# Kernel optimization log

Measured on AMD Instinct MI355X. Metric: run time of the kernel, lower is better.

## Reference

```python
import jax, jax.numpy as jnp
import numpy as np

H = 64
IN_DIM = 32
N = 50000
E = 100000
B = 500


def setup_inputs() -> dict:
    key = jax.random.key(0)
    ks = jax.random.split(key, 16)
    def rn(k, shape, s=0.05):
        return jax.random.normal(k, shape, dtype=jnp.float32) * s
    inp = dict(
        nfeat=rn(ks[0], (N, IN_DIM), 1.0),
        efeat=rn(ks[1], (E, 5), 1.0),
        lin0_w=rn(ks[2], (IN_DIM, H)), lin0_b=jnp.zeros((H,), jnp.float32),
        ew1=rn(ks[3], (5, 128)), eb1=jnp.zeros((128,), jnp.float32),
        ew2=rn(ks[4], (128, H * H)), eb2=jnp.zeros((H * H,), jnp.float32),
        conv_b=jnp.zeros((H,), jnp.float32),
        gru_wih=rn(ks[5], (3 * H, H)), gru_whh=rn(ks[6], (3 * H, H)),
        gru_bih=jnp.zeros((3 * H,), jnp.float32), gru_bhh=jnp.zeros((3 * H,), jnp.float32),
        lstm_wih=rn(ks[7], (4 * H, 2 * H)), lstm_whh=rn(ks[8], (4 * H, H)),
        lstm_bih=jnp.zeros((4 * H,), jnp.float32), lstm_bhh=jnp.zeros((4 * H,), jnp.float32),
        fc1_w=rn(ks[9], (2 * H, H)), fc1_b=jnp.zeros((H,), jnp.float32),
        fc2_w=rn(ks[10], (H, 1)), fc2_b=jnp.zeros((1,), jnp.float32),
        src=jax.random.randint(ks[11], (E,), 0, N),
        dst=jax.random.randint(ks[12], (E,), 0, N),
        graph_id=jnp.arange(N) // (N // B),  # B graphs of equal size, sorted
        num_graphs=B,
    )
    return inp


def reference(nfeat, efeat, lin0_w, lin0_b, ew1, eb1, ew2, eb2, conv_b,
              gru_wih, gru_whh, gru_bih, gru_bhh,
              lstm_wih, lstm_whh, lstm_bih, lstm_bhh,
              fc1_w, fc1_b, fc2_w, fc2_b,
              src, dst, graph_id, num_graphs):
    n_nodes = nfeat.shape[0]
    # lin0 + relu
    h = jax.nn.relu(nfeat @ lin0_w + lin0_b)  # [N, H]
    # edge-conditioned weight matrices (same for all 3 iterations)
    We = (jax.nn.relu(efeat @ ew1 + eb1) @ ew2 + eb2).reshape(-1, H, H)  # [E, H, H]
    deg = jnp.maximum(
        jax.ops.segment_sum(jnp.ones(src.shape[0], jnp.float32), dst, num_segments=n_nodes), 1.0)
    for _ in range(3):
        # NNConv: gather src feats, per-edge matmul, scatter-mean at dst
        msg = jnp.einsum('eh,eho->eo', h[src], We)  # [E, H]
        agg = jax.ops.segment_sum(msg, dst, num_segments=n_nodes) / deg[:, None]
        m = jax.nn.relu(agg + conv_b)
        # GRU step (PyTorch gate order r,z,n)
        gi = m @ gru_wih.T + gru_bih
        gh = h @ gru_whh.T + gru_bhh
        r = jax.nn.sigmoid(gi[:, :H] + gh[:, :H])
        z = jax.nn.sigmoid(gi[:, H:2 * H] + gh[:, H:2 * H])
        n = jnp.tanh(gi[:, 2 * H:] + r * gh[:, 2 * H:])
        h = (1.0 - z) * n + z * h
    feat = h  # [N, H]
    # Set2Set pooling: 3 iters, 1-layer LSTM with input 2H
    q_star = jnp.zeros((num_graphs, 2 * H), jnp.float32)
    hh = jnp.zeros((num_graphs, H), jnp.float32)
    cc = jnp.zeros((num_graphs, H), jnp.float32)
    for _ in range(3):
        gates = q_star @ lstm_wih.T + lstm_bih + hh @ lstm_whh.T + lstm_bhh
        i = jax.nn.sigmoid(gates[:, :H])
        f = jax.nn.sigmoid(gates[:, H:2 * H])
        g = jnp.tanh(gates[:, 2 * H:3 * H])
        o = jax.nn.sigmoid(gates[:, 3 * H:])
        cc = f * cc + i * g
        hh = o * jnp.tanh(cc)
        q = hh  # [B, H]
        e = jnp.sum(feat * q[graph_id], axis=-1)  # [N]
        emax = jax.ops.segment_max(e, graph_id, num_segments=num_graphs)
        alpha = jnp.exp(e - emax[graph_id])
        denom = jax.ops.segment_sum(alpha, graph_id, num_segments=num_graphs)
        alpha = alpha / denom[graph_id]
        readout = jax.ops.segment_sum(alpha[:, None] * feat, graph_id, num_segments=num_graphs)
        q_star = jnp.concatenate([q, readout], axis=-1)  # [B, 2H]
    pred = jax.nn.relu(q_star @ fc1_w + fc1_b) @ fc2_w + fc2_b  # [B, 1]
    return pred.reshape(-1)
```

## Files before the change

### kernel.cpp

```cpp
#include <hip/hip_runtime.h>

#define HD 64
#define NNODE 50000
#define NEDGE 100000
#define NGR 500
#define NPG 100
#define EPAD 100352
#define NCH 66
#define NUPL 65

typedef _Float16 f16;
typedef _Float16 f16x2 __attribute__((ext_vector_type(2)));
typedef _Float16 f16x8 __attribute__((ext_vector_type(8)));
typedef float f32x4 __attribute__((ext_vector_type(4)));

__device__ __forceinline__ float sigmoidf_(float x) { return 1.f / (1.f + __expf(-x)); }

__device__ __forceinline__ void gload16(const void* g, void* l) {
    __builtin_amdgcn_global_load_lds((const __attribute__((address_space(1))) unsigned int*)g,
                                     (__attribute__((address_space(3))) unsigned int*)l, 16, 0, 0);
}

#define G_NODE 12500
#define G_EMLP 392
#define G_GRU  48
#define G_T1   128
#define G_T2   64
#define G_IDX  392
#define G_ALL (G_NODE + G_EMLP + G_GRU + G_T1 + G_T2 + G_IDX)

__global__ __launch_bounds__(256) void k_prep_all(
    const float* __restrict__ nfeat, const float* __restrict__ lin0_w, const float* __restrict__ lin0_b,
    const float* __restrict__ efeat, const float* __restrict__ ew1, const float* __restrict__ eb1,
    const float* __restrict__ gwih, const float* __restrict__ gwhh,
    const float* __restrict__ lwih, const float* __restrict__ lwhh,
    const int* __restrict__ src, const int* __restrict__ dst,
    float* __restrict__ h, f16x2* __restrict__ uP,
    f16* __restrict__ gB1, f16* __restrict__ gB2,
    float* __restrict__ lwihT, float* __restrict__ lwhhT,
    int* __restrict__ srcP, int* __restrict__ dstP, int* __restrict__ cnt) {
    int bb = blockIdx.x;
    int t = threadIdx.x;
    if (bb < G_NODE) {
        int idx = bb * 256 + t;
        int n = idx >> 6, o = idx & 63;
        if (n >= NNODE) return;
        const float* nf = nfeat + n * 32;
        float acc = lin0_b[o];
#pragma unroll
        for (int i = 0; i < 32; i++) acc += nf[i] * lin0_w[i * 64 + o];
        h[idx] = fmaxf(acc, 0.f);
        return;
    }
    bb -= G_NODE;
    if (bb < G_EMLP) {
        __shared__ float sw[5 * 128];
        __shared__ float sb[128];
        for (int idx = t; idx < 640; idx += 256) sw[idx] = ew1[idx];
        if (t < 128) sb[t] = eb1[t];
        __syncthreads();
        int e = bb * 256 + t;
        bool valid = e < NEDGE;
        float ef[5];
#pragma unroll
        for (int i = 0; i < 5; i++) ef[i] = valid ? efeat[e * 5 + i] : 0.f;
#pragma unroll 2
        for (int c = 0; c < 64; c++) {
            float v[2];
#pragma unroll
            for (int s = 0; s < 2; s++) {
                int k = 2 * c + s;
                float acc = sb[k];
#pragma unroll
                for (int i = 0; i < 5; i++) acc += ef[i] * sw[i * 128 + k];
                v[s] = valid ? fmaxf(acc, 0.f) : 0.f;
            }
            f16x2 pv;
            pv[0] = (f16)v[0];
            pv[1] = (f16)v[1];
            uP[(size_t)c * EPAD + e] = pv;
        }
        {
            f16x2 pv;
            pv[0] = valid ? (f16)1.f : (f16)0.f;
            pv[1] = pv[0];
            uP[(size_t)64 * EPAD + e] = pv;
        }
        return;
    }
    bb -= G_EMLP;
    if (bb < G_GRU) {
        int idx = bb * 256 + t;
        int cp = idx >> 6, k = idx & 63;
        int w = cp / 48, rem = cp % 48;
        int tg = rem >> 4, cc = rem & 15;
        int orow = tg * 64 + w * 16 + cc;
        gB1[idx] = (f16)gwih[orow * 64 + k];
        gB2[idx] = (f16)gwhh[orow * 64 + k];
        return;
    }
    bb -= G_GRU;
    if (bb < G_T1) {
        int idx = bb * 256 + t;
        int r = idx >> 7, c = idx & 127;
        lwihT[c * 256 + r] = lwih[idx];
        return;
    }
    bb -= G_T1;
    if (bb < G_T2) {
        int idx = bb * 256 + t;
        int r = idx >> 6, c = idx & 63;
        lwhhT[c * 256 + r] = lwhh[idx];
        return;
    }
    bb -= G_T2;
    {
        int e = bb * 256 + t;
        if (e >= EPAD) return;
        if (e < NEDGE) {
            int d = dst[e];
            srcP[e] = src[e];
            dstP[e] = d;
            atomicAdd(&cnt[d], 1);
        } else {
            srcP[e] = 0;
            dstP[e] = -1;
        }
    }
}

__global__ __launch_bounds__(256) void k_pack_b(const float* __restrict__ ew2,
                                                const float* __restrict__ eb2,
                                                f16* __restrict__ w2hp) {
    __shared__ float s[8192];
    int c = blockIdx.x, t = threadIdx.x;
    for (int i = t; i < 8192; i += 256) {
        int kg = c * 128 + (i >> 6);
        float v = 0.f;
        if (kg < 8192) v = ew2[(size_t)c * 8192 + i];
        else if (kg < 8256) v = eb2[(kg - 8192) * 64 + (i & 63)];
        s[i] = v;
    }
    __syncthreads();
    f16* outp = w2hp + (size_t)c * 8192 + t * 32;
#pragma unroll
    for (int ff = 0; ff < 4; ff++) {
        int F = t * 4 + ff;
        int l = F & 63;
        int jj = (F >> 6) & 3;
        int sl = (F >> 8) & 3;
        f16x8 v;
#pragma unroll
        for (int q = 0; q < 8; q++)
            v[q] = (f16)s[(sl * 32 + ((l >> 4) << 3) + q) * 64 + jj * 16 + (l & 15)];
        *(f16x8*)(outp + ff * 8) = v;
    }
}

__global__ __launch_bounds__(256) void k_msg(
    const float* __restrict__ h, const f16x2* __restrict__ uP, const f16* __restrict__ w2hp,
    const int* __restrict__ srcP, const int* __restrict__ dstP, float* __restrict__ agg) {
    __shared__ __attribute__((aligned(16))) f16 sB[2 * 8192];
    int t = threadIdx.x;
    int w = t >> 6, l = t & 63;
    int eb = blockIdx.x * 256 + w * 64;
    int lr = l & 15, lg = l >> 4;
    f16x8 xf[4][2];
#pragma unroll
    for (int i = 0; i < 4; i++) {
        const float* xb = h + (size_t)srcP[eb + i * 16 + lr] * 64;
#pragma unroll
        for (int p = 0; p < 2; p++) {
            float4 v0 = *(const float4*)(xb + p * 32 + lg * 8);
            float4 v1 = *(const float4*)(xb + p * 32 + lg * 8 + 4);
            f16x8 xv;
            xv[0] = (f16)v0.x; xv[1] = (f16)v0.y; xv[2] = (f16)v0.z; xv[3] = (f16)v0.w;
            xv[4] = (f16)v1.x; xv[5] = (f16)v1.y; xv[6] = (f16)v1.z; xv[7] = (f16)v1.w;
            xf[i][p] = xv;
        }
    }
    const f16x8* gB = (const f16x8*)w2hp;
    f16x8* sB8 = (f16x8*)sB;
#pragma unroll
    for (int i = 0; i < 4; i++)
        gload16(gB + i * 256 + w * 64 + l, sB8 + i * 256 + w * 64 + l);
    f32x4 acc[4][4];
#pragma unroll
    for (int i = 0; i < 4; i++)
#pragma unroll
        for (int j = 0; j < 4; j++) acc[i][j] = (f32x4){0.f, 0.f, 0.f, 0.f};
    f16x2 uc[4], un[4];
#pragma unroll
    for (int i = 0; i < 4; i++) uc[i] = uP[eb + i * 16 + lr];
    __syncthreads();
#pragma unroll 1
    for (int c = 0; c <= 64; c++) {
        int buf = c & 1;
        if (c < 64) {
            const f16x8* gs = gB + (size_t)(c + 1) * 1024;
            f16x8* ld = sB8 + (buf ^ 1) * 1024;
#pragma unroll
            for (int i = 0; i < 4; i++)
                gload16(gs + i * 256 + w * 64 + l, ld + i * 256 + w * 64 + l);
            int cn = c + 1;
#pragma unroll
            for (int i = 0; i < 4; i++) un[i] = uP[(size_t)cn * EPAD + eb + i * 16 + lr];
        }
        f16x8 bf[4][4];
#pragma unroll
        for (int s = 0; s < 4; s++)
#pragma unroll
            for (int j = 0; j < 4; j++)
                bf[s][j] = sB8[buf * 1024 + s * 256 + j * 64 + l];
        __builtin_amdgcn_s_setprio(1);
#pragma unroll
        for (int s = 0; s < 4; s++) {
#pragma unroll
            for (int i = 0; i < 4; i++) {
                f16x8 av = xf[i][s & 1] * uc[i][s >> 1];
#pragma unroll
                for (int j = 0; j < 4; j++)
                    acc[i][j] = __builtin_amdgcn_mfma_f32_16x16x32_f16(av, bf[s][j], acc[i][j], 0, 0, 0);
            }
        }
        __builtin_amdgcn_s_setprio(0);
#pragma unroll
        for (int i = 0; i < 4; i++) uc[i] = un[i];
        __syncthreads();
    }
#pragma unroll
    for (int i = 0; i < 4; i++) {
        int rb = eb + i * 16 + lg * 4;
        int4 d4 = *(const int4*)(dstP + rb);
#pragma unroll
        for (int r = 0; r < 4; r++) {
            int d = (r == 0) ? d4.x : (r == 1) ? d4.y : (r == 2) ? d4.z : d4.w;
            if (d >= 0) {
                float* ap = agg + (size_t)d * 64 + lr;
#pragma unroll
                for (int j = 0; j < 4; j++) atomicAdd(ap + j * 16, acc[i][j][r]);
            }
        }
    }
}

#define GWP 72
__global__ __launch_bounds__(256) void k_gru2(float* __restrict__ agg,
                                              const int* __restrict__ cnt,
                                              const float* __restrict__ convb,
                                              const f16* __restrict__ B1g,
                                              const f16* __restrict__ B2g,
                                              const float* __restrict__ bih,
                                              const float* __restrict__ bhh,
                                              float* __restrict__ h) {
    __shared__ f16 sM[64 * GWP];
    __shared__ f16 sH[64 * GWP];
    int t = threadIdx.x;
    int nb = blockIdx.x * 64;
    int w = t >> 6, l = t & 63, lr = l & 15, lg = l >> 4;
    f16x8 b1[2][3], b2[2][3];
#pragma unroll
    for (int kk = 0; kk < 2; kk++)
#pragma unroll
        for (int j = 0; j < 3; j++) {
            size_t off = (size_t)(w * 48 + j * 16 + lr) * 64 + kk * 32 + lg * 8;
            b1[kk][j] = *(const f16x8*)(B1g + off);
            b2[kk][j] = *(const f16x8*)(B2g + off);
        }
#pragma unroll
    for (int it = 0; it < 16; it++) {
        int idx = t + 256 * it;
        int node = idx >> 6, k = idx & 63;
        int gn = nb + node;
        float mv = 0.f, hv = 0.f;
        if (gn < NNODE) {
            size_t off = (size_t)gn * 64 + k;
            float dinv = 1.f / (float)max(cnt[gn], 1);
            mv = fmaxf(agg[off] * dinv + convb[k], 0.f);
            hv = h[off];
            agg[off] = 0.f;
        }
        sM[node * GWP + k] = (f16)mv;
        sH[node * GWP + k] = (f16)hv;
    }
    __syncthreads();
    f32x4 aih[4][3], ahh[4][3];
#pragma unroll
    for (int i = 0; i < 4; i++)
#pragma unroll
        for (int j = 0; j < 3; j++) {
            aih[i][j] = (f32x4){0.f, 0.f, 0.f, 0.f};
            ahh[i][j] = (f32x4){0.f, 0.f, 0.f, 0.f};
        }
#pragma unroll
    for (int kk = 0; kk < 2; kk++) {
        f16x8 am[4], ah[4];
#pragma unroll
        for (int i = 0; i < 4; i++) {
            am[i] = *(const f16x8*)(sM + (i * 16 + lr) * GWP + kk * 32 + lg * 8);
            ah[i] = *(const f16x8*)(sH + (i * 16 + lr) * GWP + kk * 32 + lg * 8);
        }
#pragma unroll
        for (int i = 0; i < 4; i++)
#pragma unroll
            for (int j = 0; j < 3; j++) {
                aih[i][j] = __builtin_amdgcn_mfma_f32_16x16x32_f16(am[i], b1[kk][j], aih[i][j], 0, 0, 0);
                ahh[i][j] = __builtin_amdgcn_mfma_f32_16x16x32_f16(ah[i], b2[kk][j], ahh[i][j], 0, 0, 0);
            }
    }
    float bi0 = bih[0 * 64 + w * 16 + lr], bh0 = bhh[0 * 64 + w * 16 + lr];
    float bi1 = bih[1 * 64 + w * 16 + lr], bh1 = bhh[1 * 64 + w * 16 + lr];
    float bi2 = bih[2 * 64 + w * 16 + lr], bh2 = bhh[2 * 64 + w * 16 + lr];
#pragma unroll
    for (int i = 0; i < 4; i++)
#pragma unroll
        for (int r = 0; r < 4; r++) {
            int node = i * 16 + lg * 4 + r;
            int gn = nb + node;
            if (gn >= NNODE) continue;
            float rg = sigmoidf_(aih[i][0][r] + bi0 + ahh[i][0][r] + bh0);
            float z = sigmoidf_(aih[i][1][r] + bi1 + ahh[i][1][r] + bh1);
            float nn = tanhf(aih[i][2][r] + bi2 + rg * (ahh[i][2][r] + bh2));
            size_t off = (size_t)gn * 64 + w * 16 + lr;
            float hold = h[off];
            h[off] = (1.f - z) * nn + z * hold;
        }
}

#define FP 68
__global__ __launch_bounds__(256) void k_s2s(const float* __restrict__ feat,
                                             const float* __restrict__ wihT,
                                             const float* __restrict__ whhT,
                                             const float* __restrict__ lbih,
                                             const float* __restrict__ lbhh,
                                             const float* __restrict__ fc1w,
                                             const float* __restrict__ fc1b,
                                             const float* __restrict__ fc2w,
                                             const float* __restrict__ fc2b,
                                             float* __restrict__ out) {
    __shared__ float sf[NPG * FP];
    __shared__ float sq[128];
    __shared__ float sh[64], scc[64];
    __shared__ float sg[256];
    __shared__ float se[NPG];
    __shared__ float red[2];
    int g = blockIdx.x, t = threadIdx.x;
    const float* fb = feat + (size_t)g * NPG * 64;
    for (int idx = t; idx < NPG * 64; idx += 256)
        sf[(idx >> 6) * FP + (idx & 63)] = fb[idx];
    if (t < 128) sq[t] = 0.f;
    if (t >= 128 && t < 192) { sh[t - 128] = 0.f; scc[t - 128] = 0.f; }
    __syncthreads();
    for (int it = 0; it < 3; it++) {
        float gate = lbih[t] + lbhh[t];
#pragma unroll 8
        for (int i = 0; i < 128; i++) gate += sq[i] * wihT[i * 256 + t];
#pragma unroll 8
        for (int i = 0; i < 64; i++) gate += sh[i] * whhT[i * 256 + t];
        sg[t] = gate;
        __syncthreads();
        if (t < 64) {
            float ig = sigmoidf_(sg[t]);
            float fg = sigmoidf_(sg[64 + t]);
            float gg = tanhf(sg[128 + t]);
            float og = sigmoidf_(sg[192 + t]);
            float c = fg * scc[t] + ig * gg;
            scc[t] = c;
            float hv = og * tanhf(c);
            sh[t] = hv;
            sq[t] = hv;
        }
        __syncthreads();
        if (t < NPG) {
            float e = 0.f;
#pragma unroll 8
            for (int o = 0; o < 64; o++) e += sf[t * FP + o] * sh[o];
            se[t] = e;
        }
        __syncthreads();
        if (t < 64) {
            float m = -1e30f;
            for (int i2 = t; i2 < NPG; i2 += 64) m = fmaxf(m, se[i2]);
            for (int d = 32; d; d >>= 1) m = fmaxf(m, __shfl_down(m, d));
            if (t == 0) red[0] = m;
        }
        __syncthreads();
        float emax = red[0];
        if (t < NPG) se[t] = __expf(se[t] - emax);
        __syncthreads();
        if (t < 64) {
            float s = 0.f;
            for (int i2 = t; i2 < NPG; i2 += 64) s += se[i2];
            for (int d = 32; d; d >>= 1) s += __shfl_down(s, d);
            if (t == 0) red[1] = s;
        }
        __syncthreads();
        if (t < 64) {
            float dnv = 1.f / red[1];
            float r = 0.f;
#pragma unroll 4
            for (int n = 0; n < NPG; n++) r += se[n] * sf[n * FP + t];
            sq[64 + t] = r * dnv;
        }
        __syncthreads();
    }
    if (t < 64) {
        float hsum = fc1b[t];
#pragma unroll 8
        for (int i = 0; i < 128; i++) hsum += sq[i] * fc1w[i * 64 + t];
        float p = fmaxf(hsum, 0.f) * fc2w[t];
        for (int d = 32; d; d >>= 1) p += __shfl_down(p, d);
        if (t == 0) out[g] = p + fc2b[0];
    }
}

extern "C" void kernel_launch(void* const* d_in, const int* in_sizes, int n_in,
                              void* d_out, int out_size, void* d_ws, size_t ws_size,
                              hipStream_t stream) {
    const float* nfeat = (const float*)d_in[0];
    const float* efeat = (const float*)d_in[1];
    const float* lin0_w = (const float*)d_in[2];
    const float* lin0_b = (const float*)d_in[3];
    const float* ew1 = (const float*)d_in[4];
    const float* eb1 = (const float*)d_in[5];
    const float* ew2 = (const float*)d_in[6];
    const float* eb2 = (const float*)d_in[7];
    const float* convb = (const float*)d_in[8];
    const float* gwih = (const float*)d_in[9];
    const float* gwhh = (const float*)d_in[10];
    const float* gbih = (const float*)d_in[11];
    const float* gbhh = (const float*)d_in[12];
    const float* lwih = (const float*)d_in[13];
    const float* lwhh = (const float*)d_in[14];
    const float* lbih = (const float*)d_in[15];
    const float* lbhh = (const float*)d_in[16];
    const float* fc1w = (const float*)d_in[17];
    const float* fc1b = (const float*)d_in[18];
    const float* fc2w = (const float*)d_in[19];
    const float* fc2b = (const float*)d_in[20];
    const int* src = (const int*)d_in[21];
    const int* dst = (const int*)d_in[22];
    float* out = (float*)d_out;

    char* p = (char*)d_ws;
    auto alloc = [&](size_t bytes) {
        char* q = p;
        p += (bytes + 255) & ~(size_t)255;
        return q;
    };
    f16x2* uP = (f16x2*)alloc((size_t)NUPL * EPAD * 4);
    f16* w2hp = (f16*)alloc((size_t)NCH * 8192 * 2);
    float* h = (float*)alloc((size_t)NNODE * 64 * 4);
    float* agg = (float*)alloc((size_t)NNODE * 64 * 4);
    int* cnt = (int*)alloc((size_t)NNODE * 4);
    float* lwihT = (float*)alloc((size_t)128 * 256 * 4);
    float* lwhhT = (float*)alloc((size_t)64 * 256 * 4);
    f16* gB1 = (f16*)alloc((size_t)12288 * 2);
    f16* gB2 = (f16*)alloc((size_t)12288 * 2);
    int* srcP = (int*)alloc((size_t)EPAD * 4);
    int* dstP = (int*)alloc((size_t)EPAD * 4);
    if ((size_t)(p - (char*)d_ws) > ws_size) return;

    hipMemsetAsync(cnt, 0, (size_t)NNODE * 4, stream);
    hipMemsetAsync(agg, 0, (size_t)NNODE * 64 * 4, stream);

    k_prep_all<<<G_ALL, 256, 0, stream>>>(nfeat, lin0_w, lin0_b, efeat, ew1, eb1,
                                          gwih, gwhh, lwih, lwhh, src, dst,
                                          h, uP, gB1, gB2, lwihT, lwhhT, srcP, dstP, cnt);
    k_pack_b<<<NCH, 256, 0, stream>>>(ew2, eb2, w2hp);

    for (int it = 0; it < 3; it++) {
        k_msg<<<EPAD / 256, 256, 0, stream>>>(h, uP, w2hp, srcP, dstP, agg);
        k_gru2<<<(NNODE + 63) / 64, 256, 0, stream>>>(agg, cnt, convb, gB1, gB2, gbih, gbhh, h);
    }
    k_s2s<<<NGR, 256, 0, stream>>>(h, lwihT, lwhhT, lbih, lbhh, fc1w, fc1b, fc2w, fc2b, out);
}
```

Baseline: 482.2 us.

## Process two weight chunks per k_msg stage, fold packing into prep kernel

```diff
diff --git a/kernel.cpp b/kernel.cpp
--- a/kernel.cpp
+++ b/kernel.cpp
@@ -23,22 +23,27 @@
 
 #define G_NODE 12500
 #define G_EMLP 392
+#define G_PACK 66
 #define G_GRU  48
 #define G_T1   128
 #define G_T2   64
 #define G_IDX  392
-#define G_ALL (G_NODE + G_EMLP + G_GRU + G_T1 + G_T2 + G_IDX)
+#define G_ALL (G_NODE + G_EMLP + G_PACK + G_GRU + G_T1 + G_T2 + G_IDX)
 
 __global__ __launch_bounds__(256) void k_prep_all(
     const float* __restrict__ nfeat, const float* __restrict__ lin0_w, const float* __restrict__ lin0_b,
     const float* __restrict__ efeat, const float* __restrict__ ew1, const float* __restrict__ eb1,
+    const float* __restrict__ ew2, const float* __restrict__ eb2,
     const float* __restrict__ gwih, const float* __restrict__ gwhh,
     const float* __restrict__ lwih, const float* __restrict__ lwhh,
     const int* __restrict__ src, const int* __restrict__ dst,
-    float* __restrict__ h, f16x2* __restrict__ uP,
+    float* __restrict__ h, f16x2* __restrict__ uP, f16* __restrict__ w2hp,
     f16* __restrict__ gB1, f16* __restrict__ gB2,
     float* __restrict__ lwihT, float* __restrict__ lwhhT,
     int* __restrict__ srcP, int* __restrict__ dstP, int* __restrict__ cnt) {
+    __shared__ float sw[5 * 128];
+    __shared__ float sb[128];
+    __shared__ float s[8192];
     int bb = blockIdx.x;
     int t = threadIdx.x;
     if (bb < G_NODE) {
@@ -54,8 +59,6 @@
     }
     bb -= G_NODE;
     if (bb < G_EMLP) {
-        __shared__ float sw[5 * 128];
-        __shared__ float sb[128];
         for (int idx = t; idx < 640; idx += 256) sw[idx] = ew1[idx];
         if (t < 128) sb[t] = eb1[t];
         __syncthreads();
@@ -68,12 +71,12 @@
         for (int c = 0; c < 64; c++) {
             float v[2];
 #pragma unroll
-            for (int s = 0; s < 2; s++) {
-                int k = 2 * c + s;
+            for (int ss = 0; ss < 2; ss++) {
+                int k = 2 * c + ss;
                 float acc = sb[k];
 #pragma unroll
                 for (int i = 0; i < 5; i++) acc += ef[i] * sw[i * 128 + k];
-                v[s] = valid ? fmaxf(acc, 0.f) : 0.f;
+                v[ss] = valid ? fmaxf(acc, 0.f) : 0.f;
             }
             f16x2 pv;
             pv[0] = (f16)v[0];
@@ -89,6 +92,32 @@
         return;
     }
     bb -= G_EMLP;
+    if (bb < G_PACK) {
+        int c = bb;
+        for (int i = t; i < 8192; i += 256) {
+            int kg = c * 128 + (i >> 6);
+            float v = 0.f;
+            if (kg < 8192) v = ew2[(size_t)c * 8192 + i];
+            else if (kg < 8256) v = eb2[(kg - 8192) * 64 + (i & 63)];
+            s[i] = v;
+        }
+        __syncthreads();
+        f16* outp = w2hp + (size_t)c * 8192 + t * 32;
+#pragma unroll
+        for (int ff = 0; ff < 4; ff++) {
+            int F = t * 4 + ff;
+            int l = F & 63;
+            int jj = (F >> 6) & 3;
+            int sl = (F >> 8) & 3;
+            f16x8 v;
+#pragma unroll
+            for (int q = 0; q < 8; q++)
+                v[q] = (f16)s[(sl * 32 + ((l >> 4) << 3) + q) * 64 + jj * 16 + (l & 15)];
+            *(f16x8*)(outp + ff * 8) = v;
+        }
+        return;
+    }
+    bb -= G_PACK;
     if (bb < G_GRU) {
         int idx = bb * 256 + t;
         int cp = idx >> 6, k = idx & 63;
@@ -129,38 +158,10 @@
     }
 }
 
-__global__ __launch_bounds__(256) void k_pack_b(const float* __restrict__ ew2,
-                                                const float* __restrict__ eb2,
-                                                f16* __restrict__ w2hp) {
-    __shared__ float s[8192];
-    int c = blockIdx.x, t = threadIdx.x;
-    for (int i = t; i < 8192; i += 256) {
-        int kg = c * 128 + (i >> 6);
-        float v = 0.f;
-        if (kg < 8192) v = ew2[(size_t)c * 8192 + i];
-        else if (kg < 8256) v = eb2[(kg - 8192) * 64 + (i & 63)];
-        s[i] = v;
-    }
-    __syncthreads();
-    f16* outp = w2hp + (size_t)c * 8192 + t * 32;
-#pragma unroll
-    for (int ff = 0; ff < 4; ff++) {
-        int F = t * 4 + ff;
-        int l = F & 63;
-        int jj = (F >> 6) & 3;
-        int sl = (F >> 8) & 3;
-        f16x8 v;
-#pragma unroll
-        for (int q = 0; q < 8; q++)
-            v[q] = (f16)s[(sl * 32 + ((l >> 4) << 3) + q) * 64 + jj * 16 + (l & 15)];
-        *(f16x8*)(outp + ff * 8) = v;
-    }
-}
-
 __global__ __launch_bounds__(256) void k_msg(
     const float* __restrict__ h, const f16x2* __restrict__ uP, const f16* __restrict__ w2hp,
     const int* __restrict__ srcP, const int* __restrict__ dstP, float* __restrict__ agg) {
-    __shared__ __attribute__((aligned(16))) f16 sB[2 * 8192];
+    __shared__ __attribute__((aligned(16))) f16 sB[2 * 16384];
     int t = threadIdx.x;
     int w = t >> 6, l = t & 63;
     int eb = blockIdx.x * 256 + w * 64;
@@ -182,50 +183,76 @@
     const f16x8* gB = (const f16x8*)w2hp;
     f16x8* sB8 = (f16x8*)sB;
 #pragma unroll
+    for (int i = 0; i < 8; i++)
+        gload16(gB + i * 256 + t, sB8 + i * 256 + t);
+    f32x4 acc[4][4];
+#pragma unroll
     for (int i = 0; i < 4; i++)
-        gload16(gB + i * 256 + w * 64 + l, sB8 + i * 256 + w * 64 + l);
-    f32x4 acc[4][4];
-#pragma unroll
-    for (int i = 0; i < 4; i++)
 #pragma unroll
         for (int j = 0; j < 4; j++) acc[i][j] = (f32x4){0.f, 0.f, 0.f, 0.f};
-    f16x2 uc[4], un[4];
-#pragma unroll
-    for (int i = 0; i < 4; i++) uc[i] = uP[eb + i * 16 + lr];
+    f16x2 uc0[4], uc1[4], un0[4], un1[4];
+#pragma unroll
+    for (int i = 0; i < 4; i++) {
+        uc0[i] = uP[eb + i * 16 + lr];
+        uc1[i] = uP[(size_t)EPAD + eb + i * 16 + lr];
+    }
     __syncthreads();
 #pragma unroll 1
-    for (int c = 0; c <= 64; c++) {
-        int buf = c & 1;
-        if (c < 64) {
-            const f16x8* gs = gB + (size_t)(c + 1) * 1024;
-            f16x8* ld = sB8 + (buf ^ 1) * 1024;
-#pragma unroll
-            for (int i = 0; i < 4; i++)
-                gload16(gs + i * 256 + w * 64 + l, ld + i * 256 + w * 64 + l);
-            int cn = c + 1;
-#pragma unroll
-            for (int i = 0; i < 4; i++) un[i] = uP[(size_t)cn * EPAD + eb + i * 16 + lr];
-        }
-        f16x8 bf[4][4];
-#pragma unroll
-        for (int s = 0; s < 4; s++)
-#pragma unroll
-            for (int j = 0; j < 4; j++)
-                bf[s][j] = sB8[buf * 1024 + s * 256 + j * 64 + l];
-        __builtin_amdgcn_s_setprio(1);
-#pragma unroll
-        for (int s = 0; s < 4; s++) {
+    for (int p = 0; p <= 32; p++) {
+        int buf = p & 1;
+        if (p < 32) {
+            const f16x8* gs = gB + (size_t)(p + 1) * 2048;
+            f16x8* ld = sB8 + (buf ^ 1) * 2048;
+#pragma unroll
+            for (int i = 0; i < 8; i++)
+                gload16(gs + i * 256 + t, ld + i * 256 + t);
+            int c0 = min(2 * p + 2, 64), c1 = min(2 * p + 3, 64);
 #pragma unroll
             for (int i = 0; i < 4; i++) {
-                f16x8 av = xf[i][s & 1] * uc[i][s >> 1];
+                un0[i] = uP[(size_t)c0 * EPAD + eb + i * 16 + lr];
+                un1[i] = uP[(size_t)c1 * EPAD + eb + i * 16 + lr];
+            }
+        }
+        {
+            f16x8 bf[4][4];
+#pragma unroll
+            for (int s = 0; s < 4; s++)
 #pragma unroll
                 for (int j = 0; j < 4; j++)
-                    acc[i][j] = __builtin_amdgcn_mfma_f32_16x16x32_f16(av, bf[s][j], acc[i][j], 0, 0, 0);
-            }
-        }
-        __builtin_amdgcn_s_setprio(0);
-#pragma unroll
-        for (int i = 0; i < 4; i++) uc[i] = un[i];
+                    bf[s][j] = sB8[buf * 2048 + s * 256 + j * 64 + l];
+            __builtin_amdgcn_s_setprio(1);
+#pragma unroll
+            for (int s = 0; s < 4; s++)
+#pragma unroll
+                for (int i = 0; i < 4; i++) {
+                    f16x8 av = xf[i][s & 1] * uc0[i][s >> 1];
+#pragma unroll
+                    for (int j = 0; j < 4; j++)
+                        acc[i][j] = __builtin_amdgcn_mfma_f32_16x16x32_f16(av, bf[s][j], acc[i][j], 0, 0, 0);
+                }
+            __builtin_amdgcn_s_setprio(0);
+        }
+        {
+            f16x8 bf[4][4];
+#pragma unroll
+            for (int s = 0; s < 4; s++)
+#pragma unroll
+                for (int j = 0; j < 4; j++)
+                    bf[s][j] = sB8[buf * 2048 + 1024 + s * 256 + j * 64 + l];
+            __builtin_amdgcn_s_setprio(1);
+#pragma unroll
+            for (int s = 0; s < 4; s++)
+#pragma unroll
+                for (int i = 0; i < 4; i++) {
+                    f16x8 av = xf[i][s & 1] * uc1[i][s >> 1];
+#pragma unroll
+                    for (int j = 0; j < 4; j++)
+                        acc[i][j] = __builtin_amdgcn_mfma_f32_16x16x32_f16(av, bf[s][j], acc[i][j], 0, 0, 0);
+                }
+            __builtin_amdgcn_s_setprio(0);
+        }
+#pragma unroll
+        for (int i = 0; i < 4; i++) { uc0[i] = un0[i]; uc1[i] = un1[i]; }
         __syncthreads();
     }
 #pragma unroll
@@ -252,7 +279,7 @@
                                               const f16* __restrict__ B2g,
                                               const float* __restrict__ bih,
                                               const float* __restrict__ bhh,
-                                              float* __restrict__ h) {
+                                              float* __restrict__ h, int zero_agg) {
     __shared__ f16 sM[64 * GWP];
     __shared__ f16 sH[64 * GWP];
     int t = threadIdx.x;
@@ -278,7 +305,7 @@
             float dinv = 1.f / (float)max(cnt[gn], 1);
             mv = fmaxf(agg[off] * dinv + convb[k], 0.f);
             hv = h[off];
-            agg[off] = 0.f;
+            if (zero_agg) agg[off] = 0.f;
         }
         sM[node * GWP + k] = (f16)mv;
         sH[node * GWP + k] = (f16)hv;
@@ -464,14 +491,14 @@
     hipMemsetAsync(cnt, 0, (size_t)NNODE * 4, stream);
     hipMemsetAsync(agg, 0, (size_t)NNODE * 64 * 4, stream);
 
-    k_prep_all<<<G_ALL, 256, 0, stream>>>(nfeat, lin0_w, lin0_b, efeat, ew1, eb1,
+    k_prep_all<<<G_ALL, 256, 0, stream>>>(nfeat, lin0_w, lin0_b, efeat, ew1, eb1, ew2, eb2,
                                           gwih, gwhh, lwih, lwhh, src, dst,
-                                          h, uP, gB1, gB2, lwihT, lwhhT, srcP, dstP, cnt);
-    k_pack_b<<<NCH, 256, 0, stream>>>(ew2, eb2, w2hp);
+                                          h, uP, w2hp, gB1, gB2, lwihT, lwhhT, srcP, dstP, cnt);
 
     for (int it = 0; it < 3; it++) {
         k_msg<<<EPAD / 256, 256, 0, stream>>>(h, uP, w2hp, srcP, dstP, agg);
-        k_gru2<<<(NNODE + 63) / 64, 256, 0, stream>>>(agg, cnt, convb, gB1, gB2, gbih, gbhh, h);
+        k_gru2<<<(NNODE + 63) / 64, 256, 0, stream>>>(agg, cnt, convb, gB1, gB2, gbih, gbhh, h,
+                                                      it < 2 ? 1 : 0);
     }
     k_s2s<<<NGR, 256, 0, stream>>>(h, lwihT, lwhhT, lbih, lbhh, fc1w, fc1b, fc2w, fc2b, out);
 }
```

Result: faster. 470.5 us (-2.4%).
